# Optimization experiments

Hardware: AMD Instinct MI355X
Metric: run time of the kernel (lower is better)

## Reference

```python
import jax, jax.numpy as jnp
import numpy as np

HEADS = 16

def setup_inputs() -> dict:
    key = jax.random.key(0)
    ks = jax.random.split(key, 7)
    B, S, E = 2, 2048, 1024
    return {
        "query": jax.random.normal(ks[0], (B, S, E), dtype=jnp.float32),
        "key": jax.random.normal(ks[1], (B, S, E), dtype=jnp.float32),
        "value": jax.random.normal(ks[2], (B, S, E), dtype=jnp.float32),
        "Wqkv": jax.random.normal(ks[3], (E, 3 * E), dtype=jnp.float32) * (E ** -0.5),
        "bqkv": jax.random.normal(ks[4], (3 * E,), dtype=jnp.float32) * 0.02,
        "Wproj": jax.random.normal(ks[5], (E, E), dtype=jnp.float32) * (E ** -0.5),
        "bproj": jax.random.normal(ks[6], (E,), dtype=jnp.float32) * 0.02,
    }

def reference(query, key, value, Wqkv, bqkv, Wproj, bproj):
    # key/value args are unused in the original forward (overwritten by QKV split)
    B, S, E = query.shape
    H = HEADS
    hd = E // H
    qkv = query @ Wqkv + bqkv                     # [B, S, 3E]
    qkv = qkv.reshape(B, S, H, 3 * hd).transpose(0, 2, 1, 3)  # [B, H, S, 3hd]
    q = qkv[..., :hd]
    k = qkv[..., hd:2 * hd]
    v = qkv[..., 2 * hd:]
    qk = jnp.einsum("bhqd,bhkd->bhqk", q, k)
    # faithful quirk: original divides by head_dim**-0.5, i.e. multiplies by sqrt(hd)
    scaled = qk / (hd ** -0.5)
    attn = jax.nn.softmax(scaled, axis=-1)        # dropout p=0 -> identity
    out = jnp.einsum("bhqk,bhkd->bhqd", attn, v)  # [B, H, S, hd]
    out = out.transpose(0, 2, 1, 3).reshape(B, S, E)
    return out @ Wproj + bproj
```

## Files before the change

kernel.cpp:

```cpp
#include <hip/hip_runtime.h>
#include <hip/hip_bf16.h>
#include <stdint.h>

typedef __attribute__((ext_vector_type(8))) _Float16 f16x8;
typedef __attribute__((ext_vector_type(4))) _Float16 f16x4;
typedef __attribute__((ext_vector_type(4))) float f32x4;

static constexpr int BATCH = 2;
static constexpr int SEQ = 2048;
static constexpr int EMB = 1024;
static constexpr int NH = 16;
static constexpr int HD_ = 64;

#define AS1 __attribute__((address_space(1)))
#define AS3 __attribute__((address_space(3)))

__device__ __forceinline__ void gload_lds16(const void* g, void* l) {
  __builtin_amdgcn_global_load_lds((const AS1 uint32_t*)g, (AS3 uint32_t*)l, 16, 0, 0);
}

__device__ __forceinline__ f32x4 mfma16(f16x8 a, f16x8 b, f32x4 c) {
  return __builtin_amdgcn_mfma_f32_16x16x32_f16(a, b, c, 0, 0, 0);
}

__device__ __forceinline__ f16x8 swzread(const _Float16* base, int row, int blk) {
  return *(const f16x8*)((const char*)base + row * 128 +
                         ((blk * 16) ^ ((row & 7) << 4)));
}

__global__ __launch_bounds__(256) void k_prep(const float* __restrict__ q,
                                              _Float16* __restrict__ qo,
                                              const float* __restrict__ wqkv,
                                              _Float16* __restrict__ wqkvo,
                                              const float* __restrict__ wproj,
                                              _Float16* __restrict__ wprojo) {
  __shared__ float tile[32][33];
  const int blk = blockIdx.x;
  const int t = threadIdx.x;
  if (blk < 4096) {
    const int idx = blk * 256 + t;
    float4 v = reinterpret_cast<const float4*>(q)[idx];
    const float* f = reinterpret_cast<const float*>(&v);
    _Float16 h[4];
#pragma unroll
    for (int i = 0; i < 4; ++i) h[i] = (_Float16)f[i];
    reinterpret_cast<uint2*>(qo)[idx] = *reinterpret_cast<uint2*>(h);
    return;
  }
  const float* in;
  _Float16* out;
  int R, C, bx, by;
  bool perm;
  if (blk < 4096 + 3072) {
    const int lo = blk - 4096;
    bx = lo % 96;
    by = lo / 96;
    in = wqkv; out = wqkvo; R = 1024; C = 3072; perm = true;
  } else {
    const int lo = blk - 7168;
    bx = lo & 31;
    by = lo >> 5;
    in = wproj; out = wprojo; R = 1024; C = 1024; perm = false;
  }
  const int tr = t >> 5, tc = t & 31;
  const int r0 = by * 32, c0 = bx * 32;
#pragma unroll
  for (int rr = 0; rr < 32; rr += 8)
    tile[tr + rr][tc] = in[(size_t)(r0 + tr + rr) * C + c0 + tc];
  __syncthreads();
#pragma unroll
  for (int rr = 0; rr < 32; rr += 8) {
    const int c = c0 + tr + rr;
    int d = c;
    if (perm) {
      const int h = c / 192, r = c - h * 192;
      d = (r < 64) ? h * 64 + r
                   : (r < 128 ? 1024 + h * 64 + (r - 64) : 2048 + h * 64 + (r - 128));
    }
    out[(size_t)d * R + r0 + tc] = (_Float16)tile[tc][tr + rr];
  }
}

__global__ __launch_bounds__(256) void k_gemm_qkv(const _Float16* __restrict__ A,
                                                  const _Float16* __restrict__ Bt,
                                                  const float* __restrict__ bias,
                                                  _Float16* __restrict__ oq,
                                                  _Float16* __restrict__ ok,
                                                  _Float16* __restrict__ ov) {
  constexpr int K = EMB;
  __shared__ _Float16 As[2][128 * 32];
  __shared__ _Float16 Bs[2][128 * 32];
  const int t = threadIdx.x;
  const int l = t & 63, w = t >> 6;
  const int lr = l & 15, lg = l >> 4;
  const int wr = w >> 1, wc = w & 1;
  const int m0 = blockIdx.y * 128, n0 = blockIdx.x * 128;

  auto stage = [&](int buf, int k0) {
#pragma unroll
    for (int j = 0; j < 2; ++j) {
      const int c = t + 256 * j;
      const int row = c >> 2, cb = c & 3;
      gload_lds16(A + (size_t)(m0 + row) * K + k0 + cb * 8, &As[buf][c * 8]);
      gload_lds16(Bt + (size_t)(n0 + row) * K + k0 + cb * 8, &Bs[buf][c * 8]);
    }
  };

  f32x4 acc[4][4];
#pragma unroll
  for (int m = 0; m < 4; ++m)
#pragma unroll
    for (int n = 0; n < 4; ++n) acc[m][n] = f32x4{0.f, 0.f, 0.f, 0.f};

  stage(0, 0);
  const int NT = K / 32;
  int cur = 0;
  for (int kt = 0; kt < NT; ++kt) {
    __syncthreads();
    if (kt + 1 < NT) stage(cur ^ 1, (kt + 1) * 32);
    f16x8 af[4], bf[4];
#pragma unroll
    for (int m = 0; m < 4; ++m)
      af[m] = *(const f16x8*)&As[cur][(wr * 64 + m * 16 + lr) * 32 + lg * 8];
#pragma unroll
    for (int n = 0; n < 4; ++n)
      bf[n] = *(const f16x8*)&Bs[cur][(wc * 64 + n * 16 + lr) * 32 + lg * 8];
#pragma unroll
    for (int m = 0; m < 4; ++m)
#pragma unroll
      for (int n = 0; n < 4; ++n) acc[m][n] = mfma16(af[m], bf[n], acc[m][n]);
    cur ^= 1;
  }

  const int sec = n0 >> 10;
#pragma unroll
  for (int m = 0; m < 4; ++m) {
#pragma unroll
    for (int n = 0; n < 4; ++n) {
      const int col = n0 + wc * 64 + n * 16 + lr;
      const int cc = col & 1023;
      const int h = cc >> 6, r = cc & 63;
      const float bv = bias[h * 192 + sec * 64 + r];
      const int row0 = m0 + wr * 64 + m * 16 + lg * 4;
      const int b = row0 >> 11, s0 = row0 & (SEQ - 1);
      if (sec == 2) {
        f16x4 vv;
#pragma unroll
        for (int i = 0; i < 4; ++i) vv[i] = (_Float16)(acc[m][n][i] + bv);
        *(f16x4*)&ov[(((size_t)b * NH + h) * HD_ + r) * SEQ + s0] = vv;
      } else {
#pragma unroll
        for (int i = 0; i < 4; ++i) {
          const float v = acc[m][n][i] + bv;
          const size_t dst = (((size_t)b * NH + h) * SEQ + s0 + i) * HD_ + r;
          if (sec == 0)
            oq[dst] = (_Float16)(v * 11.5415603f);
          else
            ok[dst] = (_Float16)v;
        }
      }
    }
  }
}

__global__ __launch_bounds__(256) void k_gemm_proj(const _Float16* __restrict__ A,
                                                   const _Float16* __restrict__ Bt,
                                                   const float* __restrict__ bias,
                                                   float* __restrict__ of) {
  constexpr int K = EMB, N = EMB;
  __shared__ _Float16 As[2][128 * 32];
  __shared__ _Float16 Bs[2][128 * 32];
  const int t = threadIdx.x;
  const int l = t & 63, w = t >> 6;
  const int lr = l & 15, lg = l >> 4;
  const int wr = w >> 1, wc = w & 1;
  const int m0 = blockIdx.y * 128, n0 = blockIdx.x * 128;

  auto stage = [&](int buf, int k0) {
#pragma unroll
    for (int j = 0; j < 2; ++j) {
      const int c = t + 256 * j;
      const int row = c >> 2, cb = c & 3;
      gload_lds16(A + (size_t)(m0 + row) * K + k0 + cb * 8, &As[buf][c * 8]);
      gload_lds16(Bt + (size_t)(n0 + row) * K + k0 + cb * 8, &Bs[buf][c * 8]);
    }
  };

  f32x4 acc[4][4];
#pragma unroll
  for (int m = 0; m < 4; ++m)
#pragma unroll
    for (int n = 0; n < 4; ++n) acc[m][n] = f32x4{0.f, 0.f, 0.f, 0.f};

  stage(0, 0);
  const int NT = K / 32;
  int cur = 0;
  for (int kt = 0; kt < NT; ++kt) {
    __syncthreads();
    if (kt + 1 < NT) stage(cur ^ 1, (kt + 1) * 32);
    f16x8 af[4], bf[4];
#pragma unroll
    for (int m = 0; m < 4; ++m)
      af[m] = *(const f16x8*)&As[cur][(wr * 64 + m * 16 + lr) * 32 + lg * 8];
#pragma unroll
    for (int n = 0; n < 4; ++n)
      bf[n] = *(const f16x8*)&Bs[cur][(wc * 64 + n * 16 + lr) * 32 + lg * 8];
#pragma unroll
    for (int m = 0; m < 4; ++m)
#pragma unroll
      for (int n = 0; n < 4; ++n) acc[m][n] = mfma16(af[m], bf[n], acc[m][n]);
    cur ^= 1;
  }

#pragma unroll
  for (int m = 0; m < 4; ++m)
#pragma unroll
    for (int n = 0; n < 4; ++n)
#pragma unroll
      for (int i = 0; i < 4; ++i) {
        const int row = m0 + wr * 64 + m * 16 + lg * 4 + i;
        const int col = n0 + wc * 64 + n * 16 + lr;
        of[(size_t)row * N + col] = acc[m][n][i] + bias[col];
      }
}

__global__ __launch_bounds__(512) void k_attn(
    const _Float16* __restrict__ qs, const _Float16* __restrict__ ks,
    const _Float16* __restrict__ vt, _Float16* __restrict__ op,
    float* __restrict__ marr, float* __restrict__ larr) {
  __shared__ _Float16 Kt[2][64][64];
  __shared__ _Float16 Vt[2][64][64];
  __shared__ _Float16 Plh[8][16][32];
  const int t = threadIdx.x;
  const int l = t & 63, w = t >> 6;
  const int lr = l & 15, lg = l >> 4;
  const int id = blockIdx.x;
  const int xc = id & 7, m_ = id >> 3;
  const int kvh = m_ & 1;
  const int bh = xc + 8 * (m_ >> 5);
  const int qb = ((m_ >> 1) & 15) * 128 + w * 16;
  const int kvbase = kvh * (SEQ / 2);

  const size_t qoff = ((size_t)bh * SEQ + qb + lr) * HD_;
  const f16x8 qf0 = *(const f16x8*)(qs + qoff + lg * 8);
  const f16x8 qf1 = *(const f16x8*)(qs + qoff + 32 + lg * 8);

  const _Float16* kbase = ks + (size_t)bh * SEQ * HD_;
  const _Float16* vbase = vt + (size_t)bh * HD_ * SEQ;

  const int srow = t >> 3, scb = t & 7;
  auto stage = [&](const int buf, const int kv0) {
    gload_lds16(kbase + (size_t)(kv0 + srow) * HD_ + (scb ^ (srow & 7)) * 8,
                &Kt[buf][srow][scb * 8]);
    gload_lds16(vbase + (size_t)srow * SEQ + kv0 + (scb ^ (srow & 7)) * 8,
                &Vt[buf][srow][scb * 8]);
  };

  stage(0, kvbase);

  float mr = -1e30f, lsum = 0.f;
  f32x4 oacc[4];
#pragma unroll
  for (int n = 0; n < 4; ++n) oacc[n] = f32x4{0.f, 0.f, 0.f, 0.f};

  char* plbase = (char*)&Plh[w][0][0];
  const int plswz = ((lr >> 1) & 3) << 4;

  const int NT = SEQ / 128;
  for (int it = 0; it < NT; ++it) {
    const int cur = it & 1;
    __syncthreads();
    if (it + 1 < NT) stage(cur ^ 1, kvbase + (it + 1) * 64);

    f32x4 sa[4];
    __builtin_amdgcn_s_setprio(1);
#pragma unroll
    for (int t4 = 0; t4 < 4; ++t4) {
      const int r = t4 * 16 + lr;
      const f16x8 kf0 = swzread(&Kt[cur][0][0], r, lg);
      const f16x8 kf1 = swzread(&Kt[cur][0][0], r, lg + 4);
      f32x4 s = mfma16(kf0, qf0, f32x4{0.f, 0.f, 0.f, 0.f});
      sa[t4] = mfma16(kf1, qf1, s);
    }
    __builtin_amdgcn_s_setprio(0);

    float t01 = fmaxf(fmaxf(sa[0][0], sa[0][1]), fmaxf(sa[0][2], sa[0][3]));
    float t23 = fmaxf(fmaxf(sa[1][0], sa[1][1]), fmaxf(sa[1][2], sa[1][3]));
    float t45 = fmaxf(fmaxf(sa[2][0], sa[2][1]), fmaxf(sa[2][2], sa[2][3]));
    float t67 = fmaxf(fmaxf(sa[3][0], sa[3][1]), fmaxf(sa[3][2], sa[3][3]));
    float tm = fmaxf(fmaxf(t01, t23), fmaxf(t45, t67));
    tm = fmaxf(tm, __shfl_xor(tm, 16));
    tm = fmaxf(tm, __shfl_xor(tm, 32));

    if (__all(tm < mr - 24.0f)) continue;

    if (__any(tm > mr + 8.0f)) {
      const float nm = fmaxf(mr, tm);
      const float corr = exp2f(mr - nm);
      mr = nm;
      lsum *= corr;
      float cb4[4];
#pragma unroll
      for (int i = 0; i < 4; ++i)
        cb4[i] = __shfl(corr, (l & 48) + ((l >> 4) << 2) + i);
#pragma unroll
      for (int n = 0; n < 4; ++n)
#pragma unroll
        for (int i = 0; i < 4; ++i) oacc[n][i] *= cb4[i];
    }

    float ts = 0.f;
#pragma unroll
    for (int H = 0; H < 2; ++H) {
#pragma unroll
      for (int th = 0; th < 2; ++th) {
        const int t4 = 2 * H + th;
        f16x4 pp;
#pragma unroll
        for (int i = 0; i < 4; ++i) {
          const float p = exp2f(sa[t4][i] - mr);
          ts += p;
          pp[i] = (_Float16)p;
        }
        *(f16x4*)(plbase + lr * 64 + ((th * 32 + lg * 8) ^ plswz)) = pp;
      }
      const f16x8 aP = *(const f16x8*)(plbase + lr * 64 + ((lg * 16) ^ plswz));
      __builtin_amdgcn_s_setprio(1);
#pragma unroll
      for (int n = 0; n < 4; ++n) {
        const int d = n * 16 + lr;
        const f16x8 bv = swzread(&Vt[cur][0][0], d, lg + 4 * H);
        oacc[n] = mfma16(aP, bv, oacc[n]);
      }
      __builtin_amdgcn_s_setprio(0);
    }
    ts += __shfl_xor(ts, 16);
    ts += __shfl_xor(ts, 32);
    lsum += ts;
  }

  const size_t mlbase = ((size_t)kvh * 32 + bh) * SEQ + qb;
  if (l < 16) {
    marr[mlbase + l] = mr;
    larr[mlbase + l] = lsum;
  }
  _Float16* opb = op + (size_t)kvh * BATCH * SEQ * EMB;
  const int b = bh >> 4, h = bh & 15;
#pragma unroll
  for (int n = 0; n < 4; ++n)
#pragma unroll
    for (int i = 0; i < 4; ++i) {
      const int row = qb + ((l >> 4) << 2) + i;
      opb[((size_t)b * SEQ + row) * EMB + h * HD_ + n * 16 + lr] =
          (_Float16)oacc[n][i];
    }
}

__global__ __launch_bounds__(256) void k_combine(const _Float16* __restrict__ op,
                                                 const float* __restrict__ marr,
                                                 const float* __restrict__ larr,
                                                 _Float16* __restrict__ ao) {
  const int idx = blockIdx.x * 256 + threadIdx.x;
  const int e8 = idx & 127;
  const size_t rs = (size_t)(idx >> 7);
  const int h = e8 >> 3;
  const int b = (int)(rs >> 11);
  const size_t s = rs & (SEQ - 1);
  const size_t mi = ((size_t)b * NH + h) * SEQ + s;
  const float m1 = marr[mi], l1 = larr[mi];
  const float m2 = marr[(size_t)32 * SEQ + mi], l2 = larr[(size_t)32 * SEQ + mi];
  const float mx = fmaxf(m1, m2);
  const float w1 = exp2f(m1 - mx), w2 = exp2f(m2 - mx);
  const float inv = 1.0f / (l1 * w1 + l2 * w2);
  const f16x8 o1 = ((const f16x8*)op)[idx];
  const f16x8 o2 = ((const f16x8*)op)[idx + (BATCH * SEQ * EMB / 8)];
  f16x8 r;
#pragma unroll
  for (int j = 0; j < 8; ++j)
    r[j] = (_Float16)(((float)o1[j] * w1 + (float)o2[j] * w2) * inv);
  ((f16x8*)ao)[idx] = r;
}

extern "C" void kernel_launch(void* const* d_in, const int* in_sizes, int n_in,
                              void* d_out, int out_size, void* d_ws, size_t ws_size,
                              hipStream_t stream) {
  const float* query = (const float*)d_in[0];
  const float* Wqkv = (const float*)d_in[3];
  const float* bqkv = (const float*)d_in[4];
  const float* Wproj = (const float*)d_in[5];
  const float* bproj = (const float*)d_in[6];
  float* out = (float*)d_out;

  char* ws = (char*)d_ws;
  const size_t MB = 1024 * 1024;
  _Float16* q_f16   = (_Float16*)(ws + 0);
  _Float16* Wqkv_t  = (_Float16*)(ws + 16 * MB);
  _Float16* q_s     = (_Float16*)(ws + 24 * MB);
  _Float16* k_s     = (_Float16*)(ws + 32 * MB);
  _Float16* v_t     = (_Float16*)(ws + 40 * MB);
  _Float16* op      = (_Float16*)(ws + 0);
  _Float16* Wproj_t = (_Float16*)(ws + 48 * MB);
  float*    marr    = (float*)(ws + 50 * MB);
  float*    larr    = (float*)(ws + 50 * MB + 512 * 1024);
  _Float16* a_o     = (_Float16*)(ws + 51 * MB);

  const int M = BATCH * SEQ;
  k_prep<<<dim3(8192), 256, 0, stream>>>(query, q_f16, Wqkv, Wqkv_t, Wproj, Wproj_t);
  k_gemm_qkv<<<dim3(24, M / 128), 256, 0, stream>>>(q_f16, Wqkv_t, bqkv, q_s, k_s, v_t);
  k_attn<<<dim3(1024), 512, 0, stream>>>(q_s, k_s, v_t, op, marr, larr);
  k_combine<<<dim3(BATCH * SEQ * EMB / 8 / 256), 256, 0, stream>>>(op, marr, larr, a_o);
  k_gemm_proj<<<dim3(EMB / 128, M / 128), 256, 0, stream>>>(a_o, Wproj_t, bproj, out);
}
```

Baseline: 154.1 us.

## Drop split-KV attention and combine kernel; remap QKV GEMM blocks per XCD

Attention no longer splits the KV range in two. Each block now walks the full sequence and normalizes its output by the row sum in the epilogue, so the partial-output writes, the m/l arrays and the separate combine kernel all go away. The QKV GEMM switches to a 1D grid whose index is remapped so that each XCD handles contiguous M rows, which is meant to improve L2 reuse. The trade-off is that attention launches half as many blocks, each with a loop twice as long, which lowers parallelism and occupancy.

```diff
diff --git a/kernel.cpp b/kernel.cpp
--- a/kernel.cpp
+++ b/kernel.cpp
@@ -94,7 +94,10 @@
   const int l = t & 63, w = t >> 6;
   const int lr = l & 15, lg = l >> 4;
   const int wr = w >> 1, wc = w & 1;
-  const int m0 = blockIdx.y * 128, n0 = blockIdx.x * 128;
+  const int id = blockIdx.x;
+  const int xcd = id & 7, wg = id >> 3;
+  const int m0 = (xcd * 4 + wg / 24) * 128;
+  const int n0 = (wg % 24) * 128;
 
   auto stage = [&](int buf, int k0) {
 #pragma unroll
@@ -224,10 +227,10 @@
       }
 }
 
-__global__ __launch_bounds__(512) void k_attn(
-    const _Float16* __restrict__ qs, const _Float16* __restrict__ ks,
-    const _Float16* __restrict__ vt, _Float16* __restrict__ op,
-    float* __restrict__ marr, float* __restrict__ larr) {
+__global__ __launch_bounds__(512) void k_attn(const _Float16* __restrict__ qs,
+                                              const _Float16* __restrict__ ks,
+                                              const _Float16* __restrict__ vt,
+                                              _Float16* __restrict__ ao) {
   __shared__ _Float16 Kt[2][64][64];
   __shared__ _Float16 Vt[2][64][64];
   __shared__ _Float16 Plh[8][16][32];
@@ -236,10 +239,8 @@
   const int lr = l & 15, lg = l >> 4;
   const int id = blockIdx.x;
   const int xc = id & 7, m_ = id >> 3;
-  const int kvh = m_ & 1;
-  const int bh = xc + 8 * (m_ >> 5);
-  const int qb = ((m_ >> 1) & 15) * 128 + w * 16;
-  const int kvbase = kvh * (SEQ / 2);
+  const int bh = xc + 8 * (m_ >> 4);
+  const int qb = (m_ & 15) * 128 + w * 16;
 
   const size_t qoff = ((size_t)bh * SEQ + qb + lr) * HD_;
   const f16x8 qf0 = *(const f16x8*)(qs + qoff + lg * 8);
@@ -256,7 +257,7 @@
                 &Vt[buf][srow][scb * 8]);
   };
 
-  stage(0, kvbase);
+  stage(0, 0);
 
   float mr = -1e30f, lsum = 0.f;
   f32x4 oacc[4];
@@ -266,11 +267,11 @@
   char* plbase = (char*)&Plh[w][0][0];
   const int plswz = ((lr >> 1) & 3) << 4;
 
-  const int NT = SEQ / 128;
+  const int NT = SEQ / 64;
   for (int it = 0; it < NT; ++it) {
     const int cur = it & 1;
     __syncthreads();
-    if (it + 1 < NT) stage(cur ^ 1, kvbase + (it + 1) * 64);
+    if (it + 1 < NT) stage(cur ^ 1, (it + 1) * 64);
 
     f32x4 sa[4];
     __builtin_amdgcn_s_setprio(1);
@@ -339,46 +340,19 @@
     lsum += ts;
   }
 
-  const size_t mlbase = ((size_t)kvh * 32 + bh) * SEQ + qb;
-  if (l < 16) {
-    marr[mlbase + l] = mr;
-    larr[mlbase + l] = lsum;
-  }
-  _Float16* opb = op + (size_t)kvh * BATCH * SEQ * EMB;
+  float ls4[4];
+#pragma unroll
+  for (int i = 0; i < 4; ++i)
+    ls4[i] = __shfl(lsum, (l & 48) + ((l >> 4) << 2) + i);
   const int b = bh >> 4, h = bh & 15;
 #pragma unroll
   for (int n = 0; n < 4; ++n)
 #pragma unroll
     for (int i = 0; i < 4; ++i) {
       const int row = qb + ((l >> 4) << 2) + i;
-      opb[((size_t)b * SEQ + row) * EMB + h * HD_ + n * 16 + lr] =
-          (_Float16)oacc[n][i];
-    }
-}
-
-__global__ __launch_bounds__(256) void k_combine(const _Float16* __restrict__ op,
-                                                 const float* __restrict__ marr,
-                                                 const float* __restrict__ larr,
-                                                 _Float16* __restrict__ ao) {
-  const int idx = blockIdx.x * 256 + threadIdx.x;
-  const int e8 = idx & 127;
-  const size_t rs = (size_t)(idx >> 7);
-  const int h = e8 >> 3;
-  const int b = (int)(rs >> 11);
-  const size_t s = rs & (SEQ - 1);
-  const size_t mi = ((size_t)b * NH + h) * SEQ + s;
-  const float m1 = marr[mi], l1 = larr[mi];
-  const float m2 = marr[(size_t)32 * SEQ + mi], l2 = larr[(size_t)32 * SEQ + mi];
-  const float mx = fmaxf(m1, m2);
-  const float w1 = exp2f(m1 - mx), w2 = exp2f(m2 - mx);
-  const float inv = 1.0f / (l1 * w1 + l2 * w2);
-  const f16x8 o1 = ((const f16x8*)op)[idx];
-  const f16x8 o2 = ((const f16x8*)op)[idx + (BATCH * SEQ * EMB / 8)];
-  f16x8 r;
-#pragma unroll
-  for (int j = 0; j < 8; ++j)
-    r[j] = (_Float16)(((float)o1[j] * w1 + (float)o2[j] * w2) * inv);
-  ((f16x8*)ao)[idx] = r;
+      ao[((size_t)b * SEQ + row) * EMB + h * HD_ + n * 16 + lr] =
+          (_Float16)(oacc[n][i] / ls4[i]);
+    }
 }
 
 extern "C" void kernel_launch(void* const* d_in, const int* in_sizes, int n_in,
@@ -398,16 +372,12 @@
   _Float16* q_s     = (_Float16*)(ws + 24 * MB);
   _Float16* k_s     = (_Float16*)(ws + 32 * MB);
   _Float16* v_t     = (_Float16*)(ws + 40 * MB);
-  _Float16* op      = (_Float16*)(ws + 0);
   _Float16* Wproj_t = (_Float16*)(ws + 48 * MB);
-  float*    marr    = (float*)(ws + 50 * MB);
-  float*    larr    = (float*)(ws + 50 * MB + 512 * 1024);
   _Float16* a_o     = (_Float16*)(ws + 51 * MB);
 
   const int M = BATCH * SEQ;
   k_prep<<<dim3(8192), 256, 0, stream>>>(query, q_f16, Wqkv, Wqkv_t, Wproj, Wproj_t);
-  k_gemm_qkv<<<dim3(24, M / 128), 256, 0, stream>>>(q_f16, Wqkv_t, bqkv, q_s, k_s, v_t);
-  k_attn<<<dim3(1024), 512, 0, stream>>>(q_s, k_s, v_t, op, marr, larr);
-  k_combine<<<dim3(BATCH * SEQ * EMB / 8 / 256), 256, 0, stream>>>(op, marr, larr, a_o);
+  k_gemm_qkv<<<dim3(768), 256, 0, stream>>>(q_f16, Wqkv_t, bqkv, q_s, k_s, v_t);
+  k_attn<<<dim3(512), 512, 0, stream>>>(q_s, k_s, v_t, a_o);
   k_gemm_proj<<<dim3(EMB / 128, M / 128), 256, 0, stream>>>(a_o, Wproj_t, bproj, out);
 }
```

Measured after the change: 147.9 us. 4.0% less time.
